# Performance work log

Hardware: AMD Instinct MI355X
Metric: run time of the kernel (lower is better)

## Reference

```python
import jax, jax.numpy as jnp
import numpy as np

B, T, IN = 256, 512, 256
L, C, H = 8, 16, 512
TAU = 0.1  # default temp in forward
IN0 = IN + L * C  # lstm layer-0 input size


def setup_inputs() -> dict:
    key = jax.random.key(0)
    ks = jax.random.split(key, 11)
    s = 1.0 / np.sqrt(H)  # torch LSTM/Linear uniform bound; use as std
    f32 = jnp.float32
    return {
        "states": jax.random.normal(ks[0], (B, T, IN), f32),
        "W_ih0": jax.random.normal(ks[1], (4 * H, IN0), f32) * s,
        "W_hh0": jax.random.normal(ks[2], (4 * H, H), f32) * s,
        "b_ih0": jax.random.normal(ks[3], (4 * H,), f32) * s,
        "b_hh0": jax.random.normal(ks[4], (4 * H,), f32) * s,
        "W_ih1": jax.random.normal(ks[5], (4 * H, H), f32) * s,
        "W_hh1": jax.random.normal(ks[6], (4 * H, H), f32) * s,
        "b_ih1": jax.random.normal(ks[7], (4 * H,), f32) * s,
        "b_hh1": jax.random.normal(ks[8], (4 * H,), f32) * s,
        "W_lin": jax.random.normal(ks[9], (L * C, H), f32) * s,
        # original inits linear bias to c_t[0,0,:] = one-hot(0) tiled L times
        "b_lin": jnp.tile(jnp.eye(C, dtype=f32)[0], L),
    }


def _lstm_cell(x, h, c, Wih, Whh, bih, bhh):
    # torch gate order: i, f, g, o
    g = x @ Wih.T + bih + h @ Whh.T + bhh
    i, f, gg, o = jnp.split(g, 4, axis=-1)
    c_new = jax.nn.sigmoid(f) * c + jax.nn.sigmoid(i) * jnp.tanh(gg)
    h_new = jax.nn.sigmoid(o) * jnp.tanh(c_new)
    return h_new, c_new


def reference(states, W_ih0, W_hh0, b_ih0, b_hh0, W_ih1, W_hh1, b_ih1, b_hh1, W_lin, b_lin):
    # pre-sampled gumbel noise, one draw per step (fixed key -> deterministic)
    noise = jax.random.gumbel(jax.random.key(42), (T, B, L, C), jnp.float32)
    ct0 = jnp.tile(jnp.eye(C, dtype=states.dtype)[0], (B, L))  # [B, L*C]
    h0 = jnp.zeros((2, B, H), states.dtype)
    c0 = jnp.zeros((2, B, H), states.dtype)

    def step(carry, inp):
        h, c, ct = carry
        # original detaches hidden_cell and c_t every step
        h = jax.lax.stop_gradient(h)
        c = jax.lax.stop_gradient(c)
        ct_d = jax.lax.stop_gradient(ct)
        x, g = inp  # x: [B, IN], g: [B, L, C]
        x0 = jnp.concatenate([x, ct_d], axis=-1)  # [B, IN0]
        h0n, c0n = _lstm_cell(x0, h[0], c[0], W_ih0, W_hh0, b_ih0, b_hh0)
        h1n, c1n = _lstm_cell(h0n, h[1], c[1], W_ih1, W_hh1, b_ih1, b_hh1)
        q = h1n @ W_lin.T + b_lin  # [B, L*C]
        # soft gumbel-softmax (module is in training mode -> hard=False)
        y = jax.nn.softmax((q.reshape(B, L, C) + g) / TAU, axis=-1)
        ct_new = y.reshape(B, L * C)
        new_carry = (jnp.stack([h0n, h1n]), jnp.stack([c0n, c1n]), ct_new)
        return new_carry, ct_new

    xs = (jnp.swapaxes(states, 0, 1), noise)  # time-major
    _, outs = jax.lax.scan(step, (h0, c0, ct0), xs)  # [T, B, L*C]
    return jnp.swapaxes(outs, 0, 1)  # [B, T, L*C]
```

## Files before the change

kernel.cpp:

```cpp
#include <hip/hip_runtime.h>
#include <cstdint>
#include <cstddef>

#define BB 256
#define TT 512
#define HH 512

typedef _Float16 f16;
typedef _Float16 f16x8 __attribute__((ext_vector_type(8)));
typedef float f32x4 __attribute__((ext_vector_type(4)));

__device__ __forceinline__ void tf_round(uint32_t& x0, uint32_t& x1, const int r) {
  x0 += x1;
  x1 = (x1 << r) | (x1 >> (32 - r));
  x1 ^= x0;
}

__device__ __forceinline__ void threefry2x32(uint32_t c0, uint32_t c1, uint32_t& o0, uint32_t& o1) {
  const uint32_t ks0 = 0u, ks1 = 42u;
  const uint32_t ks2 = 0x1BD11BDAu ^ ks0 ^ ks1;
  uint32_t x0 = c0 + ks0, x1 = c1 + ks1;
  tf_round(x0,x1,13); tf_round(x0,x1,15); tf_round(x0,x1,26); tf_round(x0,x1,6);
  x0 += ks1; x1 += ks2 + 1u;
  tf_round(x0,x1,17); tf_round(x0,x1,29); tf_round(x0,x1,16); tf_round(x0,x1,24);
  x0 += ks2; x1 += ks0 + 2u;
  tf_round(x0,x1,13); tf_round(x0,x1,15); tf_round(x0,x1,26); tf_round(x0,x1,6);
  x0 += ks0; x1 += ks1 + 3u;
  tf_round(x0,x1,17); tf_round(x0,x1,29); tf_round(x0,x1,16); tf_round(x0,x1,24);
  x0 += ks1; x1 += ks2 + 4u;
  tf_round(x0,x1,13); tf_round(x0,x1,15); tf_round(x0,x1,26); tf_round(x0,x1,6);
  x0 += ks2; x1 += ks0 + 5u;
  o0 = x0; o1 = x1;
}

__device__ __forceinline__ float gumbel_noise(uint32_t idx, bool fast) {
  uint32_t o0, o1;
  threefry2x32(0u, idx, o0, o1);
  uint32_t bits = o0 ^ o1;
  uint32_t fb = (bits >> 9) | 0x3f800000u;
  float u = __uint_as_float(fb) - 1.0f;
  const float tiny = 1.17549435e-38f;
  u = fmaxf(tiny, u + tiny);
  if (fast) return -__logf(-__logf(u));
  return -logf(-logf(u));
}

__device__ __forceinline__ float fsig(float x) {
  return __builtin_amdgcn_rcpf(1.0f + __expf(-x));
}
__device__ __forceinline__ float ftanh(float x) {
  float xx = fminf(fmaxf(x, -15.f), 15.f);
  float t = __expf(2.f * xx);
  return (t - 1.f) * __builtin_amdgcn_rcpf(t + 1.f);
}

__device__ __forceinline__ uint32_t aload32(const uint32_t* p) {
  return __hip_atomic_load(p, __ATOMIC_RELAXED, __HIP_MEMORY_SCOPE_AGENT);
}
__device__ __forceinline__ void astore32(uint32_t* p, uint32_t v) {
  __hip_atomic_store(p, v, __ATOMIC_RELAXED, __HIP_MEMORY_SCOPE_AGENT);
}

__device__ __forceinline__ f16x8 cvt8(f32x4 a, f32x4 b) {
  f16x8 w;
  w[0]=(f16)a[0]; w[1]=(f16)a[1]; w[2]=(f16)a[2]; w[3]=(f16)a[3];
  w[4]=(f16)b[0]; w[5]=(f16)b[1]; w[6]=(f16)b[2]; w[7]=(f16)b[3];
  return w;
}

#define MFMA_PAIR(AE, AO, WROW, KOFF) { \
  f16x8 be_ = *(const f16x8*)&(WROW)[(KOFF) + kg]; \
  f16x8 bo_ = *(const f16x8*)&(WROW)[(KOFF) + 32 + kg]; \
  acce = __builtin_amdgcn_mfma_f32_16x16x32_f16((AE), be_, acce, 0, 0, 0); \
  acco = __builtin_amdgcn_mfma_f32_16x16x32_f16((AO), bo_, acco, 0, 0, 0); }

template<bool PRE>
__global__ __launch_bounds__(512, 1) void persistent_kernel(
    const float* __restrict__ states,
    const float* __restrict__ Wih0, const float* __restrict__ Whh0,
    const float* __restrict__ bih0, const float* __restrict__ bhh0,
    const float* __restrict__ Wih1, const float* __restrict__ Whh1,
    const float* __restrict__ bih1, const float* __restrict__ bhh1,
    const float* __restrict__ Wlin, const float* __restrict__ blin,
    float* __restrict__ out,
    uint32_t* cnt0, uint32_t* flagsA, uint32_t* flagsB,
    f16* h0blk, f16* h1blk, f16* Wlc, float* noise_pre, f16* xf16)
{
  __shared__ __align__(16) f16 W0s[32][904];
  __shared__ __align__(16) f16 W1s[32][1032];
  __shared__ __align__(16) f16 ctl[64][136];
  __shared__ __align__(16) f16 hstg[16][520];
  __shared__ float bls[2][4][8];
  float (*glds)[37] = reinterpret_cast<float(*)[37]>(&hstg[0][0]);

  const int tid = threadIdx.x;
  const int bid = blockIdx.x;
  const int m = bid & 3;
  const int s = bid >> 2;
  const int lane = tid & 63;
  const int wv = tid >> 6;
  const int mu = wv >> 1;
  const int nu = wv & 1;
  const int ra = lane & 15;
  const int kg = (lane >> 4) << 3;
  const int crow = (lane >> 4) << 2;
  const int arow = mu * 16 + ra;
  const int cw = wv * 16;
  const int erow = tid >> 2;
  const int hc2 = tid & 3;

  {
    const int lc = tid & 31;
    const int gr = ((lc >> 3) << 9) + s*8 + (lc & 7);
    for (int k = tid >> 5; k < 896; k += 16) {
      float v;
      if (k < 256)      v = Wih0[(size_t)gr * 384 + k];
      else if (k < 768) v = Whh0[(size_t)gr * 512 + (k - 256)];
      else              v = Wih0[(size_t)gr * 384 + 256 + (k - 768)];
      W0s[lc][k] = (f16)v;
    }
    for (int k = tid >> 5; k < 1024; k += 16) {
      float v = (k < 512) ? Whh1[(size_t)gr * 512 + k]
                          : Wih1[(size_t)gr * 512 + (k - 512)];
      W1s[lc][k] = (f16)v;
    }
  }
  for (int e = tid; e < 64 * 128; e += 512)
    ctl[e >> 7][e & 127] = (f16)(((e & 15) == 0) ? 1.f : 0.f);
  if (tid < 64) {
    const int l = tid >> 5, g = (tid >> 3) & 3, hc = tid & 7;
    const int col = g * 512 + s*8 + hc;
    bls[l][g][hc] = l ? (bih1[col] + bhh1[col]) : (bih0[col] + bhh0[col]);
  }

  if (tid < 128) {
    const int e2 = bid * 128 + tid;
    union { f16 h[2]; uint32_t u; } pk2;
    pk2.h[0] = (f16)Wlin[2*e2]; pk2.h[1] = (f16)Wlin[2*e2 + 1];
    ((uint32_t*)Wlc)[e2] = pk2.u;
  }
  if (PRE) {
    const uint32_t base = (uint32_t)bid * 65536u;
    for (uint32_t e = tid; e < 65536u; e += 512u)
      noise_pre[base + e] = gumbel_noise(base + e, false);
    #pragma unroll
    for (int tt2 = 0; tt2 < 2; ++tt2) {
      const int tx = bid * 2 + tt2;
      const int r = tid >> 3;
      const int kb = (tid & 7) * 32;
      #pragma unroll
      for (int mm = 0; mm < 4; ++mm) {
        const float* src = states + ((size_t)(mm*64 + r) * TT + tx) * 256 + kb;
        f16* dst = xf16 + ((size_t)tx*4 + mm) * 16384;
        #pragma unroll
        for (int j = 0; j < 4; ++j) {
          f32x4 a = *(const f32x4*)(src + j*8);
          f32x4 b = *(const f32x4*)(src + j*8 + 4);
          *(f16x8*)(dst + (size_t)((kb + j*8) >> 3) * 512 + r*8) = cvt8(a, b);
        }
      }
    }
  }
  __syncthreads();
  if (tid == 0) {
    __hip_atomic_fetch_add(cnt0, 1u, __ATOMIC_RELEASE, __HIP_MEMORY_SCOPE_AGENT);
    int g = 0;
    while (aload32(cnt0) < 256u && g < 2000000) { __builtin_amdgcn_s_sleep(1); ++g; }
    (void)__hip_atomic_load(cnt0, __ATOMIC_ACQUIRE, __HIP_MEMORY_SCOPE_AGENT);
  }
  __syncthreads();

  const float blq = blin[cw + ra];
  float c0a = 0.f, c0b = 0.f, c1a = 0.f, c1b = 0.f;

  f16x8 h0p[16], h1cf[16];
  #pragma unroll
  for (int q_ = 0; q_ < 16; ++q_) { h0p[q_] = f16x8{}; h1cf[q_] = f16x8{}; }
  f32x4 acce, acco;

  auto vwait = [&](uint32_t* base) {
    if (tid < 64) {
      int g = 0;
      for (;;) {
        uint32_t v = aload32(base + tid);
        if (__ballot(v != 0u) == ~0ull) break;
        if (++g > 1000000) break;
        __builtin_amdgcn_s_sleep(2);
      }
    }
    asm volatile("" ::: "memory");
    __syncthreads();
  };

  auto stage_quarter = [&](const f16* slab, int q) {
    const f16* src = slab + q * 8192;
    f16x8 a = *(const f16x8*)(src + tid*8);
    f16x8 b = *(const f16x8*)(src + 4096 + tid*8);
    *(f16x8*)&hstg[tid >> 6][(tid & 63) * 8] = a;
    *(f16x8*)&hstg[8 + (tid >> 6)][(tid & 63) * 8] = b;
  };
  auto lfrag = [&](int row, int kloc) -> f16x8 {
    return *(const f16x8*)&hstg[kloc >> 3][row * 8];
  };

  auto q_phase = [&](int tq) {
    float nzq[4][4];
    if (PRE) {
      const float* np0 = noise_pre + ((size_t)tq*256 + m*64 + crow) * 128 + cw + ra;
      #pragma unroll
      for (int mu2 = 0; mu2 < 4; ++mu2)
        #pragma unroll
        for (int r = 0; r < 4; ++r)
          nzq[mu2][r] = np0[(size_t)(mu2*16 + r) * 128];
    }
    vwait(flagsB + (size_t)(tq*4 + m) * 64);
    const f16* hb = h1blk + ((size_t)tq*4 + m) * 32768;
    f32x4 accq[4] = {{0,0,0,0},{0,0,0,0},{0,0,0,0},{0,0,0,0}};
    #pragma unroll
    for (int q = 0; q < 4; ++q) {
      if (q) __syncthreads();
      stage_quarter(hb, q);
      __syncthreads();
      h1cf[4*q]     = lfrag(arow, kg);
      h1cf[4*q + 1] = lfrag(arow, 32 + kg);
      h1cf[4*q + 2] = lfrag(arow, 64 + kg);
      h1cf[4*q + 3] = lfrag(arow, 96 + kg);
      #pragma unroll
      for (int jj = 0; jj < 2; ++jj) {
        const f16* wqp = Wlc + (size_t)(cw + ra) * 512 + (q*2 + jj) * 64;
        f16x8 bE = *(const f16x8*)(wqp + kg);
        f16x8 bO = *(const f16x8*)(wqp + 32 + kg);
        #pragma unroll
        for (int mu2 = 0; mu2 < 4; ++mu2) {
          f16x8 ae = lfrag(mu2*16 + ra, jj*64 + kg);
          f16x8 ao = lfrag(mu2*16 + ra, jj*64 + 32 + kg);
          accq[mu2] = __builtin_amdgcn_mfma_f32_16x16x32_f16(ae, bE, accq[mu2], 0, 0, 0);
          accq[mu2] = __builtin_amdgcn_mfma_f32_16x16x32_f16(ao, bO, accq[mu2], 0, 0, 0);
        }
      }
    }
    __syncthreads();
    #pragma unroll
    for (int mu2 = 0; mu2 < 4; ++mu2) {
      #pragma unroll
      for (int r = 0; r < 4; ++r) {
        const int row = mu2*16 + crow + r;
        const int col = cw + ra;
        float g;
        if (PRE) g = nzq[mu2][r];
        else g = gumbel_noise(((uint32_t)tq*256u + (uint32_t)(m*64 + row)) * 128u + (uint32_t)col, true);
        float v = (accq[mu2][r] + blq + g) * 10.0f;
        float mx = v;
        #pragma unroll
        for (int k_ = 1; k_ < 16; k_ <<= 1) mx = fmaxf(mx, __shfl_xor(mx, k_));
        float ex = __expf(v - mx);
        float sm = ex;
        #pragma unroll
        for (int k_ = 1; k_ < 16; k_ <<= 1) sm += __shfl_xor(sm, k_);
        ctl[row][col] = (f16)(ex * __builtin_amdgcn_rcpf(sm));
      }
    }
    __syncthreads();
    if (tid < 128)
      out[((size_t)(m*64 + s) * TT + tq) * 128 + tid] = (float)ctl[s][tid];
  };

  auto epilogue = [&](int L, float& ca, float& cb, f16* blkbuf, int t, uint32_t* slot) {
    f32x4 av = acce + acco;
    #pragma unroll
    for (int r = 0; r < 4; ++r)
      glds[mu*16 + crow + r][nu*16 + ra] = av[r];
    __syncthreads();
    if (tid < 256) {
      const int h2 = hc2 * 2;
      float ia = glds[erow][h2]      + bls[L][0][h2];
      float ib = glds[erow][h2 + 1]  + bls[L][0][h2 + 1];
      float fa = glds[erow][8 + h2]  + bls[L][1][h2];
      float fb = glds[erow][9 + h2]  + bls[L][1][h2 + 1];
      float ga = glds[erow][16 + h2] + bls[L][2][h2];
      float gb = glds[erow][17 + h2] + bls[L][2][h2 + 1];
      float oa = glds[erow][24 + h2] + bls[L][3][h2];
      float ob = glds[erow][25 + h2] + bls[L][3][h2 + 1];
      float cna = fsig(fa) * ca + fsig(ia) * ftanh(ga);
      float cnb = fsig(fb) * cb + fsig(ib) * ftanh(gb);
      ca = cna; cb = cnb;
      union { f16 h[2]; uint32_t u; } pk;
      pk.h[0] = (f16)(fsig(oa) * ftanh(cna));
      pk.h[1] = (f16)(fsig(ob) * ftanh(cnb));
      uint32_t* pb = (uint32_t*)(blkbuf + ((size_t)t*4 + m) * 32768 + (size_t)s * 512);
      astore32(pb + erow*4 + hc2, pk.u);
    }
    asm volatile("s_waitcnt vmcnt(0)" ::: "memory");
    __syncthreads();
    if (tid == 0) astore32(slot, 1u);
  };

  for (int t = 0; t < TT; ++t) {
    f16x8 xe[4], xo[4];
    if (PRE) {
      const f16* xb16 = xf16 + ((size_t)t*4 + m) * 16384;
      #pragma unroll
      for (int j = 0; j < 4; ++j) {
        xe[j] = *(const f16x8*)(xb16 + (size_t)((j*64 + kg) >> 3) * 512 + arow*8);
        xo[j] = *(const f16x8*)(xb16 + (size_t)((j*64 + 32 + kg) >> 3) * 512 + arow*8);
      }
    } else {
      const float* xb = states + ((size_t)(m*64 + arow) * TT + t) * 256;
      #pragma unroll
      for (int j = 0; j < 4; ++j) {
        f32x4 a0 = *(const f32x4*)(xb + j*64 + kg);
        f32x4 a1 = *(const f32x4*)(xb + j*64 + kg + 4);
        f32x4 b0 = *(const f32x4*)(xb + j*64 + 32 + kg);
        f32x4 b1 = *(const f32x4*)(xb + j*64 + 32 + kg + 4);
        xe[j] = cvt8(a0, a1);
        xo[j] = cvt8(b0, b1);
      }
    }

    acce = f32x4{0,0,0,0}; acco = f32x4{0,0,0,0};
    #pragma unroll
    for (int j = 0; j < 4; ++j)
      MFMA_PAIR(xe[j], xo[j], W0s[nu*16 + ra], j*64)
    #pragma unroll
    for (int j = 4; j < 12; ++j)
      MFMA_PAIR(h0p[2*(j-4)], h0p[2*(j-4) + 1], W0s[nu*16 + ra], j*64)

    if (t > 0) q_phase(t - 1);

    {
      f16x8 ae = *(const f16x8*)&ctl[arow][kg];
      f16x8 ao = *(const f16x8*)&ctl[arow][32 + kg];
      MFMA_PAIR(ae, ao, W0s[nu*16 + ra], 768)
      ae = *(const f16x8*)&ctl[arow][64 + kg];
      ao = *(const f16x8*)&ctl[arow][96 + kg];
      MFMA_PAIR(ae, ao, W0s[nu*16 + ra], 832)
    }
    epilogue(0, c0a, c0b, h0blk, t, flagsA + (size_t)(t*4 + m)*64 + s);

    acce = f32x4{0,0,0,0}; acco = f32x4{0,0,0,0};
    #pragma unroll
    for (int j = 0; j < 8; ++j)
      MFMA_PAIR(h1cf[2*j], h1cf[2*j + 1], W1s[nu*16 + ra], j*64)

    vwait(flagsA + (size_t)(t*4 + m)*64);
    {
      const f16* hb0 = h0blk + ((size_t)t*4 + m) * 32768;
      #pragma unroll
      for (int q = 0; q < 4; ++q) {
        __syncthreads();
        stage_quarter(hb0, q);
        __syncthreads();
        h0p[4*q]     = lfrag(arow, kg);
        h0p[4*q + 1] = lfrag(arow, 32 + kg);
        h0p[4*q + 2] = lfrag(arow, 64 + kg);
        h0p[4*q + 3] = lfrag(arow, 96 + kg);
        MFMA_PAIR(h0p[4*q],     h0p[4*q + 1], W1s[nu*16 + ra], (8 + 2*q)*64)
        MFMA_PAIR(h0p[4*q + 2], h0p[4*q + 3], W1s[nu*16 + ra], (9 + 2*q)*64)
      }
    }
    __syncthreads();
    epilogue(1, c1a, c1b, h1blk, t, flagsB + (size_t)(t*4 + m)*64 + s);
  }

  q_phase(TT - 1);
}

extern "C" void kernel_launch(void* const* d_in, const int* in_sizes, int n_in,
                              void* d_out, int out_size, void* d_ws, size_t ws_size,
                              hipStream_t stream) {
  const float* states = (const float*)d_in[0];
  const float* Wih0 = (const float*)d_in[1];
  const float* Whh0 = (const float*)d_in[2];
  const float* bih0 = (const float*)d_in[3];
  const float* bhh0 = (const float*)d_in[4];
  const float* Wih1 = (const float*)d_in[5];
  const float* Whh1 = (const float*)d_in[6];
  const float* bih1 = (const float*)d_in[7];
  const float* bhh1 = (const float*)d_in[8];
  const float* Wlin = (const float*)d_in[9];
  const float* blin = (const float*)d_in[10];
  float* out = (float*)d_out;
  (void)in_sizes; (void)n_in; (void)out_size;

  char* ws = (char*)d_ws;
  uint32_t* flagsA = (uint32_t*)ws;
  uint32_t* flagsB = (uint32_t*)(ws + 524288);
  uint32_t* cnt0   = (uint32_t*)(ws + 1048576);
  const size_t cnt_bytes = 1048832;
  f16* Wlc = (f16*)(ws + cnt_bytes);
  char* p = ws + cnt_bytes + 131072;

  f16* h0b = (f16*)p;
  f16* h1b = (f16*)(p + 134217728ull);
  float* noise = (float*)(p + 2ull*134217728);
  f16* xf16 = (f16*)(p + 2ull*134217728 + 67108864);

  const size_t need1 = cnt_bytes + 131072 + 2ull*134217728;
  const size_t need2 = need1 + 2ull*67108864;

  hipMemsetAsync(ws, 0, cnt_bytes, stream);
  if (ws_size >= need2) {
    persistent_kernel<true><<<256, 512, 0, stream>>>(
        states, Wih0, Whh0, bih0, bhh0, Wih1, Whh1, bih1, bhh1, Wlin, blin,
        out, cnt0, flagsA, flagsB, h0b, h1b, Wlc, noise, xf16);
  } else {
    persistent_kernel<false><<<256, 512, 0, stream>>>(
        states, Wih0, Whh0, bih0, bhh0, Wih1, Whh1, bih1, bhh1, Wlin, blin,
        out, cnt0, flagsA, flagsB, h0b, h1b, Wlc, nullptr, nullptr);
  }
}
```

Measured before the change: 8.223 ms.

## Prefetch next-step inputs and read h0 fragments directly from global memory

The next timestep's x inputs are now loaded early, after the layer-0 epilogue, so their global latency overlaps the layer-1 work. The layer-1 h0 operand fragments are read straight from global memory into registers instead of being staged through LDS with pairs of __syncthreads. The q-phase issues all four h1 quarter loads up front before the LDS staging loop. Together these aim to cut serialized global-load latency and barriers on the recurrent critical path, at the cost of extra live registers and possible occupancy pressure.

```diff
diff --git a/kernel.cpp b/kernel.cpp
--- a/kernel.cpp
+++ b/kernel.cpp
@@ -176,6 +176,7 @@
   f16x8 h0p[16], h1cf[16];
   #pragma unroll
   for (int q_ = 0; q_ < 16; ++q_) { h0p[q_] = f16x8{}; h1cf[q_] = f16x8{}; }
+  f16x8 xe[4], xo[4], xen[4], xon[4];
   f32x4 acce, acco;
 
   auto vwait = [&](uint32_t* base) {
@@ -192,15 +193,32 @@
     __syncthreads();
   };
 
-  auto stage_quarter = [&](const f16* slab, int q) {
-    const f16* src = slab + q * 8192;
-    f16x8 a = *(const f16x8*)(src + tid*8);
-    f16x8 b = *(const f16x8*)(src + 4096 + tid*8);
-    *(f16x8*)&hstg[tid >> 6][(tid & 63) * 8] = a;
-    *(f16x8*)&hstg[8 + (tid >> 6)][(tid & 63) * 8] = b;
-  };
   auto lfrag = [&](int row, int kloc) -> f16x8 {
     return *(const f16x8*)&hstg[kloc >> 3][row * 8];
+  };
+  auto hfrag = [&](const f16* bs, int k) -> f16x8 {
+    return *(const f16x8*)(bs + ((size_t)(k >> 3) * 512 + arow * 8));
+  };
+  auto load_x = [&](int t, f16x8* e, f16x8* o) {
+    if (PRE) {
+      const f16* xb16 = xf16 + ((size_t)t*4 + m) * 16384;
+      #pragma unroll
+      for (int j = 0; j < 4; ++j) {
+        e[j] = *(const f16x8*)(xb16 + (size_t)((j*64 + kg) >> 3) * 512 + arow*8);
+        o[j] = *(const f16x8*)(xb16 + (size_t)((j*64 + 32 + kg) >> 3) * 512 + arow*8);
+      }
+    } else {
+      const float* xb = states + ((size_t)(m*64 + arow) * TT + t) * 256;
+      #pragma unroll
+      for (int j = 0; j < 4; ++j) {
+        f32x4 a0 = *(const f32x4*)(xb + j*64 + kg);
+        f32x4 a1 = *(const f32x4*)(xb + j*64 + kg + 4);
+        f32x4 b0 = *(const f32x4*)(xb + j*64 + 32 + kg);
+        f32x4 b1 = *(const f32x4*)(xb + j*64 + 32 + kg + 4);
+        e[j] = cvt8(a0, a1);
+        o[j] = cvt8(b0, b1);
+      }
+    }
   };
 
   auto q_phase = [&](int tq) {
@@ -215,11 +233,18 @@
     }
     vwait(flagsB + (size_t)(tq*4 + m) * 64);
     const f16* hb = h1blk + ((size_t)tq*4 + m) * 32768;
+    f16x8 qreg[8];
+    #pragma unroll
+    for (int q = 0; q < 4; ++q) {
+      qreg[2*q]     = *(const f16x8*)(hb + q*8192 + tid*8);
+      qreg[2*q + 1] = *(const f16x8*)(hb + q*8192 + 4096 + tid*8);
+    }
     f32x4 accq[4] = {{0,0,0,0},{0,0,0,0},{0,0,0,0},{0,0,0,0}};
     #pragma unroll
     for (int q = 0; q < 4; ++q) {
       if (q) __syncthreads();
-      stage_quarter(hb, q);
+      *(f16x8*)&hstg[tid >> 6][(tid & 63) * 8]       = qreg[2*q];
+      *(f16x8*)&hstg[8 + (tid >> 6)][(tid & 63) * 8] = qreg[2*q + 1];
       __syncthreads();
       h1cf[4*q]     = lfrag(arow, kg);
       h1cf[4*q + 1] = lfrag(arow, 32 + kg);
@@ -295,28 +320,9 @@
     if (tid == 0) astore32(slot, 1u);
   };
 
+  load_x(0, xe, xo);
+
   for (int t = 0; t < TT; ++t) {
-    f16x8 xe[4], xo[4];
-    if (PRE) {
-      const f16* xb16 = xf16 + ((size_t)t*4 + m) * 16384;
-      #pragma unroll
-      for (int j = 0; j < 4; ++j) {
-        xe[j] = *(const f16x8*)(xb16 + (size_t)((j*64 + kg) >> 3) * 512 + arow*8);
-        xo[j] = *(const f16x8*)(xb16 + (size_t)((j*64 + 32 + kg) >> 3) * 512 + arow*8);
-      }
-    } else {
-      const float* xb = states + ((size_t)(m*64 + arow) * TT + t) * 256;
-      #pragma unroll
-      for (int j = 0; j < 4; ++j) {
-        f32x4 a0 = *(const f32x4*)(xb + j*64 + kg);
-        f32x4 a1 = *(const f32x4*)(xb + j*64 + kg + 4);
-        f32x4 b0 = *(const f32x4*)(xb + j*64 + 32 + kg);
-        f32x4 b1 = *(const f32x4*)(xb + j*64 + 32 + kg + 4);
-        xe[j] = cvt8(a0, a1);
-        xo[j] = cvt8(b0, b1);
-      }
-    }
-
     acce = f32x4{0,0,0,0}; acco = f32x4{0,0,0,0};
     #pragma unroll
     for (int j = 0; j < 4; ++j)
@@ -337,6 +343,11 @@
     }
     epilogue(0, c0a, c0b, h0blk, t, flagsA + (size_t)(t*4 + m)*64 + s);
 
+    {
+      const int tn = (t + 1 < TT) ? t + 1 : t;
+      load_x(tn, xen, xon);
+    }
+
     acce = f32x4{0,0,0,0}; acco = f32x4{0,0,0,0};
     #pragma unroll
     for (int j = 0; j < 8; ++j)
@@ -346,20 +357,19 @@
     {
       const f16* hb0 = h0blk + ((size_t)t*4 + m) * 32768;
       #pragma unroll
-      for (int q = 0; q < 4; ++q) {
-        __syncthreads();
-        stage_quarter(hb0, q);
-        __syncthreads();
-        h0p[4*q]     = lfrag(arow, kg);
-        h0p[4*q + 1] = lfrag(arow, 32 + kg);
-        h0p[4*q + 2] = lfrag(arow, 64 + kg);
-        h0p[4*q + 3] = lfrag(arow, 96 + kg);
-        MFMA_PAIR(h0p[4*q],     h0p[4*q + 1], W1s[nu*16 + ra], (8 + 2*q)*64)
-        MFMA_PAIR(h0p[4*q + 2], h0p[4*q + 3], W1s[nu*16 + ra], (9 + 2*q)*64)
-      }
-    }
-    __syncthreads();
+      for (int j = 0; j < 8; ++j) {
+        h0p[2*j]     = hfrag(hb0, j*64 + kg);
+        h0p[2*j + 1] = hfrag(hb0, j*64 + 32 + kg);
+      }
+    }
+    #pragma unroll
+    for (int j = 8; j < 16; ++j)
+      MFMA_PAIR(h0p[2*(j-8)], h0p[2*(j-8) + 1], W1s[nu*16 + ra], j*64)
+
     epilogue(1, c1a, c1b, h1blk, t, flagsB + (size_t)(t*4 + m)*64 + s);
+
+    #pragma unroll
+    for (int j = 0; j < 4; ++j) { xe[j] = xen[j]; xo[j] = xon[j]; }
   }
 
   q_phase(TT - 1);
```

Measured after the change: 6.813 ms. 17.1% less time.
